# Kernel optimization log

Hardware: AMD Instinct MI355X
Metric: run time of the kernel (lower is better)

## Reference

```python
import jax, jax.numpy as jnp
import numpy as np

H = 512  # hidden_size


def setup_inputs() -> dict:
    key = jax.random.key(0)
    ks = jax.random.split(key, 12)
    B, E, S, V = 64, 512, 400, 50000
    s = 1.0 / np.sqrt(H)
    inp = {
        'embedded': jax.random.normal(ks[0], (B, E), jnp.float32),
        'hidden': jax.random.normal(ks[1], (1, B, H), jnp.float32),
        'encoder_states': jax.random.normal(ks[2], (S, B, H), jnp.float32),
        # GRU params (PyTorch layout: gates ordered r,z,n)
        'w_ih': jax.random.uniform(ks[3], (3 * H, E), jnp.float32, -s, s),
        'w_hh': jax.random.uniform(ks[4], (3 * H, H), jnp.float32, -s, s),
        'b_ih': jax.random.uniform(ks[5], (3 * H,), jnp.float32, -s, s),
        'b_hh': jax.random.uniform(ks[6], (3 * H,), jnp.float32, -s, s),
        # nn.Bilinear(H, H, 1)
        'bilin_w': jax.random.uniform(ks[7], (1, H, H), jnp.float32, -s, s),
        'bilin_b': jax.random.uniform(ks[8], (1,), jnp.float32, -s, s),
        # out: Linear(2H, V)
        'out_w': jax.random.uniform(ks[9], (V, 2 * H), jnp.float32, -1.0 / np.sqrt(2 * H), 1.0 / np.sqrt(2 * H)),
        'out_b': jax.random.uniform(ks[10], (V,), jnp.float32, -1.0 / np.sqrt(2 * H), 1.0 / np.sqrt(2 * H)),
    }
    return inp


def reference(embedded, hidden, encoder_states, w_ih, w_hh, b_ih, b_hh,
              bilin_w, bilin_b, out_w, out_b):
    h0 = hidden[0]                                   # [B, H]
    # --- single-step GRU cell (PyTorch gate order r, z, n) ---
    gi = embedded @ w_ih.T + b_ih                    # [B, 3H]
    gh = h0 @ w_hh.T + b_hh                          # [B, 3H]
    r = jax.nn.sigmoid(gi[:, :H] + gh[:, :H])
    z = jax.nn.sigmoid(gi[:, H:2 * H] + gh[:, H:2 * H])
    n = jnp.tanh(gi[:, 2 * H:] + r * gh[:, 2 * H:])
    h_new = (1.0 - z) * n + z * h0                   # [B, H]
    # --- bilinear attention: energy[s,b] = h_new[b] @ W @ enc[s,b] + bias ---
    tmp = h_new @ bilin_w[0]                         # [B, H]
    energy = jnp.einsum('bh,sbh->sb', tmp, encoder_states) + bilin_b[0]  # [S, B]
    attn = jax.nn.softmax(energy, axis=0)            # softmax over source positions
    context = jnp.einsum('sb,sbh->bh', attn, encoder_states)             # [B, H]
    combined = jnp.concatenate([h_new, context], axis=1)                 # [B, 2H]
    logits = combined @ out_w.T + out_b              # [B, V]
    logp = jax.nn.log_softmax(logits, axis=1)
    return logp, h_new[None], attn[:, :, None]
```

## Files before the change

kernel.cpp:

```cpp
#include <hip/hip_runtime.h>
#include <math.h>

static constexpr int H = 512;
static constexpr int B = 64;
static constexpr int FP = 8;

typedef __bf16 bf16x8 __attribute__((ext_vector_type(8)));
typedef __bf16 bf16x4 __attribute__((ext_vector_type(4)));
typedef float f32x4 __attribute__((ext_vector_type(4)));

__device__ __forceinline__ float sigmoidf_(float x) { return 1.f / (1.f + expf(-x)); }

__global__ __launch_bounds__(256) void gemm_gigh(
    const float* __restrict__ embedded, const float* __restrict__ hidden,
    const float* __restrict__ w_ih, const float* __restrict__ w_hh,
    float* __restrict__ gi, float* __restrict__ gh, int K, int N)
{
    const float* A = blockIdx.y ? hidden : embedded;
    const float* W = blockIdx.y ? w_hh : w_ih;
    float* C       = blockIdx.y ? gh : gi;

    __shared__ __bf16 As[2][64 * 64];
    __shared__ __bf16 Ws[2][64 * 64];

    const int tid  = threadIdx.x;
    const int lane = tid & 63;
    const int wv   = tid >> 6;
    const int n0   = blockIdx.x * 64;
    const int lrow = tid >> 2;
    const int lq   = tid & 3;

    const float* Aptr = A + (size_t)lrow * K + lq * 16;
    const float* Wptr = W + (size_t)(n0 + lrow) * K + lq * 16;

    f32x4 acc[4] = {};
    float4 ra[4], rw[4];
    #pragma unroll
    for (int i = 0; i < 4; ++i) {
        ra[i] = *(const float4*)(Aptr + 4 * i);
        rw[i] = *(const float4*)(Wptr + 4 * i);
    }

    const int ln = lane & 15;
    const int lk = (lane >> 4) << 3;
    const int NT = K >> 6;

    for (int t = 0; t < NT; ++t) {
        __bf16* a_s = As[t & 1];
        __bf16* w_s = Ws[t & 1];
        #pragma unroll
        for (int i = 0; i < 4; ++i) {
            const int off = ((lrow << 6) + lq * 16 + 4 * i) ^ ((lrow & 7) << 3);
            *(bf16x4*)&a_s[off] = bf16x4{ (__bf16)ra[i].x, (__bf16)ra[i].y, (__bf16)ra[i].z, (__bf16)ra[i].w };
            *(bf16x4*)&w_s[off] = bf16x4{ (__bf16)rw[i].x, (__bf16)rw[i].y, (__bf16)rw[i].z, (__bf16)rw[i].w };
        }
        __syncthreads();
        if (t + 1 < NT) {
            const float* Ap = Aptr + (t + 1) * 64;
            const float* Wp = Wptr + (t + 1) * 64;
            #pragma unroll
            for (int i = 0; i < 4; ++i) {
                ra[i] = *(const float4*)(Ap + 4 * i);
                rw[i] = *(const float4*)(Wp + 4 * i);
            }
        }
        bf16x8 bfrag[2];
        #pragma unroll
        for (int ks = 0; ks < 2; ++ks) {
            const int row = wv * 16 + ln;
            const int off = ((row << 6) + ks * 32 + lk) ^ ((row & 7) << 3);
            bfrag[ks] = *(bf16x8*)&w_s[off];
        }
        #pragma unroll
        for (int m = 0; m < 4; ++m) {
            const int row = m * 16 + ln;
            #pragma unroll
            for (int ks = 0; ks < 2; ++ks) {
                const int off = ((row << 6) + ks * 32 + lk) ^ ((row & 7) << 3);
                bf16x8 afrag = *(bf16x8*)&a_s[off];
                acc[m] = __builtin_amdgcn_mfma_f32_16x16x32_bf16(afrag, bfrag[ks], acc[m], 0, 0, 0);
            }
        }
    }

    const int col = n0 + wv * 16 + ln;
    #pragma unroll
    for (int m = 0; m < 4; ++m) {
        const int rbase = m * 16 + (lane >> 4) * 4;
        #pragma unroll
        for (int j = 0; j < 4; ++j)
            C[(size_t)(rbase + j) * N + col] = acc[m][j];
    }
}

__global__ __launch_bounds__(512) void gru_gates(
    const float* __restrict__ gi, const float* __restrict__ gh,
    const float* __restrict__ b_ih, const float* __restrict__ b_hh,
    const float* __restrict__ h0, float* __restrict__ hnew,
    __bf16* __restrict__ cbf)
{
    const int b = blockIdx.x;
    const int h = threadIdx.x;
    const size_t o = (size_t)b * 3 * H;
    const float r = sigmoidf_(gi[o + h] + gh[o + h] + b_ih[h] + b_hh[h]);
    const float z = sigmoidf_(gi[o + H + h] + gh[o + H + h] + b_ih[H + h] + b_hh[H + h]);
    const float n = tanhf(gi[o + 2 * H + h] + b_ih[2 * H + h]
                          + r * (gh[o + 2 * H + h] + b_hh[2 * H + h]));
    const float hn = (1.f - z) * n + z * h0[(size_t)b * H + h];
    hnew[(size_t)b * H + h] = hn;
    cbf[(size_t)b * 2 * H + h] = (__bf16)hn;
}

__global__ __launch_bounds__(256) void gemm_a64_kn(
    const float* __restrict__ A, const float* __restrict__ W,
    float* __restrict__ C, int K, int N, int ldc)
{
    __shared__ float As[64][68];
    __shared__ float Bs[64][68];
    const int tid = threadIdx.x;
    const int n0 = blockIdx.x * 64;
    const int tv = tid & 15;
    const int tb = tid >> 4;
    const int lrow = tid >> 2;
    const int lk0  = (tid & 3) * 16;

    float acc[4][4] = {{0.f, 0.f, 0.f, 0.f}};

    for (int kc = 0; kc < K; kc += 64) {
        #pragma unroll
        for (int i = 0; i < 4; ++i) {
            const float4 a = *(const float4*)(A + (size_t)lrow * K + kc + lk0 + 4 * i);
            As[lk0 + 4 * i + 0][lrow] = a.x;
            As[lk0 + 4 * i + 1][lrow] = a.y;
            As[lk0 + 4 * i + 2][lrow] = a.z;
            As[lk0 + 4 * i + 3][lrow] = a.w;
        }
        {
            const int v  = tid & 63;
            const int kg = tid >> 6;
            #pragma unroll
            for (int i = 0; i < 16; ++i) {
                const int kk = kg * 16 + i;
                Bs[kk][v] = (n0 + v < N) ? W[(size_t)(kc + kk) * N + n0 + v] : 0.f;
            }
        }
        __syncthreads();
        #pragma unroll 16
        for (int kk = 0; kk < 64; ++kk) {
            const float4 a = *(const float4*)&As[kk][tb * 4];
            const float4 b = *(const float4*)&Bs[kk][tv * 4];
            acc[0][0] += a.x * b.x; acc[0][1] += a.x * b.y; acc[0][2] += a.x * b.z; acc[0][3] += a.x * b.w;
            acc[1][0] += a.y * b.x; acc[1][1] += a.y * b.y; acc[1][2] += a.y * b.z; acc[1][3] += a.y * b.w;
            acc[2][0] += a.z * b.x; acc[2][1] += a.z * b.y; acc[2][2] += a.z * b.z; acc[2][3] += a.z * b.w;
            acc[3][0] += a.w * b.x; acc[3][1] += a.w * b.y; acc[3][2] += a.w * b.z; acc[3][3] += a.w * b.w;
        }
        __syncthreads();
    }
    #pragma unroll
    for (int i = 0; i < 4; ++i) {
        const int bb = tb * 4 + i;
        #pragma unroll
        for (int j = 0; j < 4; ++j) {
            const int n = n0 + tv * 4 + j;
            if (n < N) C[(size_t)bb * ldc + n] = acc[i][j];
        }
    }
}

__global__ __launch_bounds__(256) void flash4(
    const float* __restrict__ tmp, const float* __restrict__ enc,
    const float* __restrict__ bilin_b, float* __restrict__ energy,
    float* __restrict__ ctxp, float* __restrict__ mp, float* __restrict__ lp,
    int S)
{
    const int b  = blockIdx.x;
    const int p  = blockIdx.y;
    const int wv = threadIdx.x >> 6;
    const int ln = threadIdx.x & 63;
    const int chunk = (S + FP - 1) / FP;
    const int s0 = p * chunk;
    int s1 = s0 + chunk; if (s1 > S) s1 = S;
    const int k0 = ln * 8;

    const float4 t0 = *(const float4*)(tmp + (size_t)b * H + k0);
    const float4 t1 = *(const float4*)(tmp + (size_t)b * H + k0 + 4);
    const float bb = bilin_b[0];

    float m = -1e30f, l = 0.f;
    float4 c0 = {0.f, 0.f, 0.f, 0.f}, c1 = {0.f, 0.f, 0.f, 0.f};

    for (int s = s0 + wv; s < s1; s += 4) {
        const float* e = enc + ((size_t)s * B + b) * H + k0;
        const float4 e0 = *(const float4*)(e);
        const float4 e1 = *(const float4*)(e + 4);
        float d = e0.x * t0.x + e0.y * t0.y + e0.z * t0.z + e0.w * t0.w
                + e1.x * t1.x + e1.y * t1.y + e1.z * t1.z + e1.w * t1.w;
        #pragma unroll
        for (int off = 32; off; off >>= 1) d += __shfl_xor(d, off);
        const float E = d + bb;
        if (ln == 0) energy[(size_t)s * B + b] = E;
        const float mn = fmaxf(m, E);
        const float sc = expf(m - mn);
        const float w  = expf(E - mn);
        l = l * sc + w;
        c0.x = c0.x * sc + w * e0.x; c0.y = c0.y * sc + w * e0.y;
        c0.z = c0.z * sc + w * e0.z; c0.w = c0.w * sc + w * e0.w;
        c1.x = c1.x * sc + w * e1.x; c1.y = c1.y * sc + w * e1.y;
        c1.z = c1.z * sc + w * e1.z; c1.w = c1.w * sc + w * e1.w;
        m = mn;
    }

    __shared__ float sctx[4][H];
    __shared__ float sm4[4], sl4[4];
    *(float4*)&sctx[wv][k0]     = c0;
    *(float4*)&sctx[wv][k0 + 4] = c1;
    if (ln == 0) { sm4[wv] = m; sl4[wv] = l; }
    __syncthreads();
    const float bm = fmaxf(fmaxf(sm4[0], sm4[1]), fmaxf(sm4[2], sm4[3]));
    const float s0c = expf(sm4[0] - bm), s1c = expf(sm4[1] - bm);
    const float s2c = expf(sm4[2] - bm), s3c = expf(sm4[3] - bm);
    const float bl = sl4[0] * s0c + sl4[1] * s1c + sl4[2] * s2c + sl4[3] * s3c;
    for (int e = threadIdx.x; e < H; e += 256) {
        const float v = sctx[0][e] * s0c + sctx[1][e] * s1c
                      + sctx[2][e] * s2c + sctx[3][e] * s3c;
        ctxp[((size_t)b * FP + p) * H + e] = v;
    }
    if (threadIdx.x == 0) { mp[b * FP + p] = bm; lp[b * FP + p] = bl; }
}

__global__ __launch_bounds__(256) void attn_combine(
    const float* __restrict__ mp, const float* __restrict__ lp,
    const float* __restrict__ ctxp, const float* __restrict__ energy,
    __bf16* __restrict__ cbf, float* __restrict__ attn, int S)
{
    const int b = blockIdx.x;
    const int t = threadIdx.x;
    __shared__ float sc_[FP];
    __shared__ float sM, sInvL;
    if (t == 0) {
        float M = -1e30f;
        #pragma unroll
        for (int p = 0; p < FP; ++p) M = fmaxf(M, mp[b * FP + p]);
        float L = 0.f;
        #pragma unroll
        for (int p = 0; p < FP; ++p) {
            const float s = expf(mp[b * FP + p] - M);
            sc_[p] = s;
            L += lp[b * FP + p] * s;
        }
        sM = M; sInvL = 1.f / L;
    }
    __syncthreads();
    const float M = sM, invL = sInvL;

    for (int e = t; e < H; e += 256) {
        float acc = 0.f;
        #pragma unroll
        for (int p = 0; p < FP; ++p)
            acc += ctxp[((size_t)b * FP + p) * H + e] * sc_[p];
        cbf[(size_t)b * 2 * H + H + e] = (__bf16)(acc * invL);
    }
    for (int s = t; s < S; s += 256)
        attn[(size_t)s * B + b] = expf(energy[(size_t)s * B + b] - M) * invL;
}

__global__ __launch_bounds__(256) void gemm_big(
    const __bf16* __restrict__ Ab,
    const float* __restrict__ W,
    const float* __restrict__ bias,
    float* __restrict__ C, float* __restrict__ pm, float* __restrict__ ps,
    int N, int ldc)
{
    constexpr int K = 1024;
    __shared__ __bf16 As[64 * 256];

    const int tid  = threadIdx.x;
    const int lane = tid & 63;
    const int wv   = tid >> 6;
    const int n0   = blockIdx.x * 64 + wv * 16;
    const int ln   = lane & 15;
    const int lk8  = (lane >> 4) << 3;

    int wr = n0 + ln;
    if (wr > N - 1) wr = N - 1;
    const float* wp = W + (size_t)wr * K + lk8;

    f32x4 acc[4] = {};

    for (int q = 0; q < 4; ++q) {
        bf16x8 av[8];
        #pragma unroll
        for (int i = 0; i < 8; ++i) {
            const int c   = tid + (i << 8);
            const int row = c >> 5;
            const int eb  = (c & 31) << 3;
            av[i] = *(const bf16x8*)(Ab + (size_t)row * K + q * 256 + eb);
        }
        float4 wb[16];
        const float* wq = wp + q * 256;
        #pragma unroll
        for (int ks = 0; ks < 8; ++ks) {
            wb[2 * ks]     = *(const float4*)(wq + ks * 32);
            wb[2 * ks + 1] = *(const float4*)(wq + ks * 32 + 4);
        }
        __syncthreads();
        #pragma unroll
        for (int i = 0; i < 8; ++i) {
            const int c   = tid + (i << 8);
            const int row = c >> 5;
            const int eb  = (c & 31) << 3;
            const int off = (row << 8) + (eb ^ ((row & 7) << 3));
            *(bf16x8*)&As[off] = av[i];
        }
        __syncthreads();
        #pragma unroll
        for (int ks = 0; ks < 8; ++ks) {
            const float4 w0 = wb[2 * ks];
            const float4 w1 = wb[2 * ks + 1];
            const bf16x8 bw = { (__bf16)w0.x, (__bf16)w0.y, (__bf16)w0.z, (__bf16)w0.w,
                                (__bf16)w1.x, (__bf16)w1.y, (__bf16)w1.z, (__bf16)w1.w };
            #pragma unroll
            for (int m = 0; m < 4; ++m) {
                const int row = m * 16 + ln;
                const int off = (row << 8) + ((ks * 32 + lk8) ^ ((row & 7) << 3));
                const bf16x8 af = *(const bf16x8*)&As[off];
                acc[m] = __builtin_amdgcn_mfma_f32_16x16x32_bf16(af, bw, acc[m], 0, 0, 0);
            }
        }
    }

    const int col = n0 + ln;
    const float bv = (col < N) ? bias[col] : 0.f;
    __syncthreads();
    float* wmf = (float*)As;
    float* wsf = wmf + 256;

    #pragma unroll
    for (int m = 0; m < 4; ++m) {
        #pragma unroll
        for (int j = 0; j < 4; ++j) {
            const int rr = m * 16 + (lane >> 4) * 4 + j;
            float v = acc[m][j] + bv;
            if (col < N) C[(size_t)rr * ldc + col] = v;
            else v = -1e30f;
            float vm = v;
            #pragma unroll
            for (int off = 8; off; off >>= 1) vm = fmaxf(vm, __shfl_xor(vm, off));
            float e = (col < N) ? expf(v - vm) : 0.f;
            #pragma unroll
            for (int off = 8; off; off >>= 1) e += __shfl_xor(e, off);
            if (ln == 0) {
                wmf[wv * 64 + rr] = vm;
                wsf[wv * 64 + rr] = e;
            }
        }
    }
    __syncthreads();
    if (tid < 64) {
        const float m0 = wmf[tid], m1 = wmf[64 + tid], m2 = wmf[128 + tid], m3 = wmf[192 + tid];
        const float bm = fmaxf(fmaxf(m0, m1), fmaxf(m2, m3));
        const float bs = wsf[tid] * expf(m0 - bm) + wsf[64 + tid] * expf(m1 - bm)
                       + wsf[128 + tid] * expf(m2 - bm) + wsf[192 + tid] * expf(m3 - bm);
        pm[(size_t)tid * gridDim.x + blockIdx.x] = bm;
        ps[(size_t)tid * gridDim.x + blockIdx.x] = bs;
    }
}

__global__ __launch_bounds__(256) void lsm_rowcombine(
    const float* __restrict__ pm, const float* __restrict__ ps,
    float* __restrict__ c, int NB)
{
    const int row = blockIdx.x;
    const int t = threadIdx.x;
    const float* pmr = pm + (size_t)row * NB;
    const float* psr = ps + (size_t)row * NB;
    __shared__ float sm_[4], ss_[4];

    float m = -1e30f;
    for (int i = t; i < NB; i += 256) m = fmaxf(m, pmr[i]);
    #pragma unroll
    for (int off = 32; off; off >>= 1) m = fmaxf(m, __shfl_xor(m, off));
    if ((t & 63) == 0) sm_[t >> 6] = m;
    __syncthreads();
    m = fmaxf(fmaxf(sm_[0], sm_[1]), fmaxf(sm_[2], sm_[3]));

    float s = 0.f;
    for (int i = t; i < NB; i += 256) s += psr[i] * expf(pmr[i] - m);
    #pragma unroll
    for (int off = 32; off; off >>= 1) s += __shfl_xor(s, off);
    if ((t & 63) == 0) ss_[t >> 6] = s;
    __syncthreads();
    if (t == 0) c[row] = m + logf(ss_[0] + ss_[1] + ss_[2] + ss_[3]);
}

__global__ __launch_bounds__(256) void lsm_apply(
    float* __restrict__ logits, const float* __restrict__ c, int V)
{
    const int b = blockIdx.y;
    const int i = blockIdx.x * 256 + threadIdx.x;
    const int V4 = V >> 2;
    if (i >= V4) return;
    float4* row = (float4*)(logits + (size_t)b * V);
    float4 v = row[i];
    const float cb = c[b];
    v.x -= cb; v.y -= cb; v.z -= cb; v.w -= cb;
    row[i] = v;
}

extern "C" void kernel_launch(void* const* d_in, const int* in_sizes, int n_in,
                              void* d_out, int out_size, void* d_ws, size_t ws_size,
                              hipStream_t stream)
{
    const float* embedded = (const float*)d_in[0];
    const float* hidden   = (const float*)d_in[1];
    const float* enc      = (const float*)d_in[2];
    const float* w_ih     = (const float*)d_in[3];
    const float* w_hh     = (const float*)d_in[4];
    const float* b_ih     = (const float*)d_in[5];
    const float* b_hh     = (const float*)d_in[6];
    const float* bilin_w  = (const float*)d_in[7];
    const float* bilin_b  = (const float*)d_in[8];
    const float* out_w    = (const float*)d_in[9];
    const float* out_b    = (const float*)d_in[10];
    float* out = (float*)d_out;

    const int S = in_sizes[2] / (B * H);
    const int V = in_sizes[9] / (2 * H);
    const int NB = (V + 63) / 64;

    float* logp = out;
    float* hnew = out + (size_t)B * V;
    float* attn = hnew + (size_t)B * H;

    float* ws     = (float*)d_ws;
    float* gi     = ws;
    float* gh     = gi + (size_t)B * 3 * H;
    float* tmp    = gh + (size_t)B * 3 * H;
    float* energy = tmp + (size_t)B * H;
    float* ctxp   = energy + (size_t)S * B;
    float* mp     = ctxp + (size_t)B * FP * H;
    float* lp     = mp + (size_t)B * FP;
    float* pm     = lp + (size_t)B * FP;
    float* ps     = pm + (size_t)64 * NB;
    float* cb     = ps + (size_t)64 * NB;
    __bf16* cbf   = (__bf16*)(cb + 64);

    gemm_gigh<<<dim3(24, 2), 256, 0, stream>>>(embedded, hidden, w_ih, w_hh, gi, gh, H, 3 * H);

    gru_gates<<<B, H, 0, stream>>>(gi, gh, b_ih, b_hh, hidden, hnew, cbf);

    gemm_a64_kn<<<H / 64, 256, 0, stream>>>(hnew, bilin_w, tmp, H, H, H);

    flash4<<<dim3(B, FP), 256, 0, stream>>>(tmp, enc, bilin_b, energy, ctxp, mp, lp, S);

    attn_combine<<<B, 256, 0, stream>>>(mp, lp, ctxp, energy, cbf, attn, S);

    gemm_big<<<NB, 256, 0, stream>>>(cbf, out_w, out_b, logp, pm, ps, V, V);

    lsm_rowcombine<<<B, 256, 0, stream>>>(pm, ps, cb, NB);

    lsm_apply<<<dim3((V / 4 + 255) / 256, B), 256, 0, stream>>>(logp, cb, V);
}
```

Baseline: 157.8 us.

## Split output GEMM along K into two partial buffers, fuse reduction with softmax stats

The big vocabulary projection GEMM is split into two K-halves, doubling the grid so more CUs are busy and each block streams less weight data. The partial results go to two workspace buffers, and a new kernel sums them with the bias, writes the logits, and computes per-chunk max and sum-exp for log-softmax. This adds about 2×B×V floats of extra global writes and reads plus one more launch, in exchange for more parallelism and occupancy in the weight-bandwidth-bound GEMM.

```diff
diff --git a/kernel.cpp b/kernel.cpp
--- a/kernel.cpp
+++ b/kernel.cpp
@@ -264,65 +264,68 @@
         attn[(size_t)s * B + b] = expf(energy[(size_t)s * B + b] - M) * invL;
 }
 
-__global__ __launch_bounds__(256) void gemm_big(
+__global__ __launch_bounds__(256, 5) void gemm_bigks(
     const __bf16* __restrict__ Ab,
     const float* __restrict__ W,
-    const float* __restrict__ bias,
-    float* __restrict__ C, float* __restrict__ pm, float* __restrict__ ps,
+    float* __restrict__ Cp0, float* __restrict__ Cp1,
     int N, int ldc)
 {
     constexpr int K = 1024;
-    __shared__ __bf16 As[64 * 256];
+    __shared__ __bf16 As[64 * 128];
 
     const int tid  = threadIdx.x;
     const int lane = tid & 63;
     const int wv   = tid >> 6;
-    const int n0   = blockIdx.x * 64 + wv * 16;
+    const int t    = blockIdx.x >> 1;
+    const int kh   = blockIdx.x & 1;
+    const int kb   = kh * 512;
+    const int n0   = t * 64 + wv * 16;
     const int ln   = lane & 15;
     const int lk8  = (lane >> 4) << 3;
 
     int wr = n0 + ln;
     if (wr > N - 1) wr = N - 1;
-    const float* wp = W + (size_t)wr * K + lk8;
+    const float* wq = W + (size_t)wr * K + kb + lk8;
+    float* Cp = kh ? Cp1 : Cp0;
 
     f32x4 acc[4] = {};
 
-    for (int q = 0; q < 4; ++q) {
-        bf16x8 av[8];
-        #pragma unroll
-        for (int i = 0; i < 8; ++i) {
-            const int c   = tid + (i << 8);
-            const int row = c >> 5;
-            const int eb  = (c & 31) << 3;
-            av[i] = *(const bf16x8*)(Ab + (size_t)row * K + q * 256 + eb);
-        }
-        float4 wb[16];
-        const float* wq = wp + q * 256;
-        #pragma unroll
-        for (int ks = 0; ks < 8; ++ks) {
-            wb[2 * ks]     = *(const float4*)(wq + ks * 32);
-            wb[2 * ks + 1] = *(const float4*)(wq + ks * 32 + 4);
+    #pragma unroll
+    for (int sl = 0; sl < 4; ++sl) {
+        bf16x8 av[4];
+        #pragma unroll
+        for (int i = 0; i < 4; ++i) {
+            const int c   = (i << 8) + tid;
+            const int row = c >> 4;
+            const int eb  = (c & 15) << 3;
+            av[i] = *(const bf16x8*)(Ab + (size_t)row * K + kb + sl * 128 + eb);
+        }
+        float4 wb[8];
+        #pragma unroll
+        for (int j = 0; j < 4; ++j) {
+            wb[2 * j]     = *(const float4*)(wq + (sl * 4 + j) * 32);
+            wb[2 * j + 1] = *(const float4*)(wq + (sl * 4 + j) * 32 + 4);
         }
         __syncthreads();
         #pragma unroll
-        for (int i = 0; i < 8; ++i) {
-            const int c   = tid + (i << 8);
-            const int row = c >> 5;
-            const int eb  = (c & 31) << 3;
-            const int off = (row << 8) + (eb ^ ((row & 7) << 3));
+        for (int i = 0; i < 4; ++i) {
+            const int c   = (i << 8) + tid;
+            const int row = c >> 4;
+            const int eb  = (c & 15) << 3;
+            const int off = (row << 7) + (eb ^ ((row & 7) << 3));
             *(bf16x8*)&As[off] = av[i];
         }
         __syncthreads();
         #pragma unroll
-        for (int ks = 0; ks < 8; ++ks) {
-            const float4 w0 = wb[2 * ks];
-            const float4 w1 = wb[2 * ks + 1];
+        for (int j = 0; j < 4; ++j) {
+            const float4 w0 = wb[2 * j];
+            const float4 w1 = wb[2 * j + 1];
             const bf16x8 bw = { (__bf16)w0.x, (__bf16)w0.y, (__bf16)w0.z, (__bf16)w0.w,
                                 (__bf16)w1.x, (__bf16)w1.y, (__bf16)w1.z, (__bf16)w1.w };
             #pragma unroll
             for (int m = 0; m < 4; ++m) {
                 const int row = m * 16 + ln;
-                const int off = (row << 8) + ((ks * 32 + lk8) ^ ((row & 7) << 3));
+                const int off = (row << 7) + ((j * 32 + lk8) ^ ((row & 7) << 3));
                 const bf16x8 af = *(const bf16x8*)&As[off];
                 acc[m] = __builtin_amdgcn_mfma_f32_16x16x32_bf16(af, bw, acc[m], 0, 0, 0);
             }
@@ -330,39 +333,53 @@
     }
 
     const int col = n0 + ln;
-    const float bv = (col < N) ? bias[col] : 0.f;
-    __syncthreads();
-    float* wmf = (float*)As;
-    float* wsf = wmf + 256;
-
-    #pragma unroll
-    for (int m = 0; m < 4; ++m) {
-        #pragma unroll
-        for (int j = 0; j < 4; ++j) {
-            const int rr = m * 16 + (lane >> 4) * 4 + j;
-            float v = acc[m][j] + bv;
-            if (col < N) C[(size_t)rr * ldc + col] = v;
-            else v = -1e30f;
-            float vm = v;
+    if (col < N) {
+        #pragma unroll
+        for (int m = 0; m < 4; ++m) {
+            const int rbase = m * 16 + (lane >> 4) * 4;
             #pragma unroll
-            for (int off = 8; off; off >>= 1) vm = fmaxf(vm, __shfl_xor(vm, off));
-            float e = (col < N) ? expf(v - vm) : 0.f;
-            #pragma unroll
-            for (int off = 8; off; off >>= 1) e += __shfl_xor(e, off);
-            if (ln == 0) {
-                wmf[wv * 64 + rr] = vm;
-                wsf[wv * 64 + rr] = e;
-            }
-        }
-    }
-    __syncthreads();
-    if (tid < 64) {
-        const float m0 = wmf[tid], m1 = wmf[64 + tid], m2 = wmf[128 + tid], m3 = wmf[192 + tid];
-        const float bm = fmaxf(fmaxf(m0, m1), fmaxf(m2, m3));
-        const float bs = wsf[tid] * expf(m0 - bm) + wsf[64 + tid] * expf(m1 - bm)
-                       + wsf[128 + tid] * expf(m2 - bm) + wsf[192 + tid] * expf(m3 - bm);
-        pm[(size_t)tid * gridDim.x + blockIdx.x] = bm;
-        ps[(size_t)tid * gridDim.x + blockIdx.x] = bs;
+            for (int j = 0; j < 4; ++j)
+                Cp[(size_t)(rbase + j) * ldc + col] = acc[m][j];
+        }
+    }
+}
+
+__global__ __launch_bounds__(256) void ksum_lsm(
+    const float* __restrict__ Cp0, const float* __restrict__ Cp1,
+    const float* __restrict__ bias, float* __restrict__ C,
+    float* __restrict__ pm, float* __restrict__ ps, int V, int NB2)
+{
+    const int b  = blockIdx.y;
+    const int cb = blockIdx.x;
+    const int t  = threadIdx.x;
+    const int base = cb * 1024 + t * 4;
+    __shared__ float sm_[4], ss_[4];
+
+    float4 v = {-1e30f, -1e30f, -1e30f, -1e30f};
+    const bool act = base < V;
+    if (act) {
+        const float4 p0 = *(const float4*)(Cp0 + (size_t)b * V + base);
+        const float4 p1 = *(const float4*)(Cp1 + (size_t)b * V + base);
+        const float4 bv = *(const float4*)(bias + base);
+        v.x = p0.x + p1.x + bv.x; v.y = p0.y + p1.y + bv.y;
+        v.z = p0.z + p1.z + bv.z; v.w = p0.w + p1.w + bv.w;
+        *(float4*)(C + (size_t)b * V + base) = v;
+    }
+    float m = fmaxf(fmaxf(v.x, v.y), fmaxf(v.z, v.w));
+    #pragma unroll
+    for (int off = 32; off; off >>= 1) m = fmaxf(m, __shfl_xor(m, off));
+    if ((t & 63) == 0) sm_[t >> 6] = m;
+    __syncthreads();
+    m = fmaxf(fmaxf(sm_[0], sm_[1]), fmaxf(sm_[2], sm_[3]));
+
+    float e = act ? (expf(v.x - m) + expf(v.y - m) + expf(v.z - m) + expf(v.w - m)) : 0.f;
+    #pragma unroll
+    for (int off = 32; off; off >>= 1) e += __shfl_xor(e, off);
+    if ((t & 63) == 0) ss_[t >> 6] = e;
+    __syncthreads();
+    if (t == 0) {
+        pm[(size_t)b * NB2 + cb] = m;
+        ps[(size_t)b * NB2 + cb] = ss_[0] + ss_[1] + ss_[2] + ss_[3];
     }
 }
 
@@ -427,6 +444,7 @@
     const int S = in_sizes[2] / (B * H);
     const int V = in_sizes[9] / (2 * H);
     const int NB = (V + 63) / 64;
+    const int NB2 = (V + 1023) / 1024;
 
     float* logp = out;
     float* hnew = out + (size_t)B * V;
@@ -440,9 +458,11 @@
     float* ctxp   = energy + (size_t)S * B;
     float* mp     = ctxp + (size_t)B * FP * H;
     float* lp     = mp + (size_t)B * FP;
-    float* pm     = lp + (size_t)B * FP;
-    float* ps     = pm + (size_t)64 * NB;
-    float* cb     = ps + (size_t)64 * NB;
+    float* cp0    = lp + (size_t)B * FP;
+    float* cp1    = cp0 + (size_t)B * V;
+    float* pm     = cp1 + (size_t)B * V;
+    float* ps     = pm + (size_t)64 * NB2;
+    float* cb     = ps + (size_t)64 * NB2;
     __bf16* cbf   = (__bf16*)(cb + 64);
 
     gemm_gigh<<<dim3(24, 2), 256, 0, stream>>>(embedded, hidden, w_ih, w_hh, gi, gh, H, 3 * H);
@@ -455,9 +475,11 @@
 
     attn_combine<<<B, 256, 0, stream>>>(mp, lp, ctxp, energy, cbf, attn, S);
 
-    gemm_big<<<NB, 256, 0, stream>>>(cbf, out_w, out_b, logp, pm, ps, V, V);
-
-    lsm_rowcombine<<<B, 256, 0, stream>>>(pm, ps, cb, NB);
+    gemm_bigks<<<2 * NB, 256, 0, stream>>>(cbf, out_w, cp0, cp1, V, V);
+
+    ksum_lsm<<<dim3(NB2, B), 256, 0, stream>>>(cp0, cp1, out_b, logp, pm, ps, V, NB2);
+
+    lsm_rowcombine<<<B, 256, 0, stream>>>(pm, ps, cb, NB2);
 
     lsm_apply<<<dim3((V / 4 + 255) / 256, B), 256, 0, stream>>>(logp, cb, V);
 }
```

Measured after the change: 160.1 us. No clear change (+1.5%).
